# Performance work log

Hardware: AMD Instinct MI355X
Metric: run time of the kernel (lower is better)

## Reference

```python
import jax, jax.numpy as jnp
import numpy as np

LAMBDA_SOFTMAX = 9.0
EPS = 1e-8


def _l2norm(x, axis):
    # matches torch l2norm: x / (sqrt(sum(x^2)+eps) + eps)
    n = jnp.sqrt(jnp.sum(x * x, axis=axis, keepdims=True) + EPS) + EPS
    return x / n


def setup_inputs() -> dict:
    key = jax.random.key(0)
    k1, k2, k3, k4 = jax.random.split(key, 4)
    n_img, n_cap, n_reg, n_words, d = 128, 128, 36, 48, 1024
    return {
        "img_emb": jax.random.normal(k1, (n_img, n_reg, d), jnp.float32),
        "img_mean": jax.random.normal(k2, (n_img, d), jnp.float32),
        "cap_emb": jax.random.normal(k3, (n_cap, n_words, d), jnp.float32),
        "cap_mean": jax.random.normal(k4, (n_cap, d), jnp.float32),
    }


def reference(img_emb, img_mean, cap_emb, cap_mean):
    # img_emb: [I, R, D]; cap_emb: [C, W, D]
    n_reg = img_emb.shape[1]
    n_words = cap_emb.shape[1]
    # global similarities g[c, i]
    g = cap_mean @ img_mean.T
    # raw dot products S[c, i, r, w] = img_emb[i, r] . cap_emb[c, w]
    S = jnp.einsum('ird,cwd->cirw', img_emb, cap_emb)

    # ---- t2i branch: query=cap (w), context=img (r) ----
    # original attn [i, r, w]: leaky -> l2norm over w -> softmax over r
    a = jax.nn.leaky_relu(S, 0.1)
    a = _l2norm(a, axis=3)
    a = jax.nn.softmax(LAMBDA_SOFTMAX * a, axis=2)
    ra = g[:, :, None, None] * a
    ra = ra / jnp.sum(ra, axis=2, keepdims=True)  # renormalize over source (r)
    # t2i_sim[c, i] = mean_w sum_r ra * S  (since weightedContext.cap = ra contracted with S)
    t2i = jnp.einsum('cirw,cirw->ci', ra, S) / n_words

    # ---- i2t branch: query=img (r), context=cap (w) ----
    # original attn [i, w, r]: leaky -> l2norm over r -> softmax over w
    b = jax.nn.leaky_relu(S, 0.1)
    b = _l2norm(b, axis=2)
    b = jax.nn.softmax(LAMBDA_SOFTMAX * b, axis=3)
    rb = g[:, :, None, None] * b
    rb = rb / jnp.sum(rb, axis=3, keepdims=True)  # renormalize over source (w)
    i2t = jnp.einsum('cirw,cirw->ci', rb, S) / n_reg

    # original returns [n_image, n_caption] (columns appended per caption)
    return (t2i + i2t).T
```

## Files before the change

kernel.cpp:

```cpp
#include <hip/hip_runtime.h>
#include <hip/hip_bf16.h>


#define EPSF 1e-8f
#define LAMF 9.0f

constexpr int IN = 128, CN = 128, RN = 36, WN = 48, DN = 1024;
constexpr size_t NIMG = (size_t)IN * RN * DN;

constexpr int AROWS = 4 * RN;
constexpr int BROWS = 4 * WN;
constexpr int TROWS = AROWS + BROWS;
constexpr int BUFB  = TROWS * 64;

using short8 = __attribute__((ext_vector_type(8))) short;
using f32x4  = __attribute__((ext_vector_type(4))) float;

__device__ __forceinline__ float leaky(float x) { return x > 0.f ? x : 0.1f * x; }

__device__ __forceinline__ unsigned short f2bf(float f) {
    unsigned int b = __float_as_uint(f);
    b += 0x7FFFu + ((b >> 16) & 1u);
    return (unsigned short)(b >> 16);
}

__device__ __forceinline__ void gld_lds16(const unsigned short* g, void* l) {
    __builtin_amdgcn_global_load_lds(
        (const __attribute__((address_space(1))) unsigned int*)g,
        (__attribute__((address_space(3))) unsigned int*)l,
        16, 0, 0);
}

__global__ void cvt_bf16(const float* __restrict__ in, unsigned short* __restrict__ out, int n4) {
    int idx = blockIdx.x * blockDim.x + threadIdx.x;
    if (idx >= n4) return;
    float4 v = ((const float4*)in)[idx];
    ushort4 o;
    o.x = f2bf(v.x); o.y = f2bf(v.y); o.z = f2bf(v.z); o.w = f2bf(v.w);
    ((ushort4*)out)[idx] = o;
}

__global__ __launch_bounds__(768, 6) void scan_mfma(
    const unsigned short* __restrict__ wsb,
    float* __restrict__ out)
{
    __shared__ __align__(16) unsigned char smem[61824];
    float (*sS)[RN][WN + 1] = (float (*)[RN][WN + 1])smem;
    float* sncol = (float*)(smem + 56448);
    float* snrow = (float*)(smem + 57984);
    float* scw   = (float*)(smem + 59136);
    float* scr   = (float*)(smem + 60672);

    const int t    = threadIdx.x;
    const int lane = t & 63;
    const int wid  = t >> 6;
    const int lr   = lane & 15;
    const int lg   = lane >> 4;
    const int wrt  = wid % 3;
    const int wct  = wid / 3;

    const int bi = blockIdx.x;
    const int bc = blockIdx.y;

    unsigned int soff[2];
#pragma unroll
    for (int j = 0; j < 2; ++j) {
        int g = j * 768 + t;
        int row = g >> 2, cg = g & 3;
        int sg = cg ^ ((row >> 1) & 3);
        unsigned int off;
        if (row < AROWS)
            off = (unsigned int)((bi * AROWS + row) << 10) + sg * 8;
        else
            off = (unsigned int)NIMG + (unsigned int)((bc * BROWS + (row - AROWS)) << 10) + sg * 8;
        soff[j] = off;
    }

    const int glo = ((lg ^ ((lr >> 1) & 3)) << 4);
    const int aoff = (wrt * 48 + lr) * 64 + glo;
    const int boff = (AROWS + wct * 48 + lr) * 64 + glo;

    f32x4 acc[3][3];
#pragma unroll
    for (int rt = 0; rt < 3; ++rt)
#pragma unroll
        for (int ct = 0; ct < 3; ++ct) acc[rt][ct] = (f32x4)(0.f);

    auto stage = [&](int bsel, int d0) {
        char* bufp = (char*)smem + bsel * BUFB;
        gld_lds16(wsb + soff[0] + d0, bufp + wid * 1024);
        if (t < 576)
            gld_lds16(wsb + soff[1] + d0, bufp + 12288 + wid * 1024);
    };

    stage(0, 0);

    for (int ch = 0; ch < 32; ++ch) {
        __builtin_amdgcn_s_barrier();
        if (ch < 31) {
            stage((ch & 1) ^ 1, (ch + 1) * 32);
            if (wid < 9) asm volatile("s_waitcnt vmcnt(2)" ::: "memory");
            else         asm volatile("s_waitcnt vmcnt(1)" ::: "memory");
        } else {
            asm volatile("s_waitcnt vmcnt(0)" ::: "memory");
        }
        __builtin_amdgcn_s_barrier();
        __builtin_amdgcn_sched_barrier(0);

        const char* bufp = (const char*)smem + (ch & 1) * BUFB;
        const char* ap = bufp + aoff;
        const char* bp = bufp + boff;
        short8 a0 = *(const short8*)(ap);
        short8 a1 = *(const short8*)(ap + 1024);
        short8 a2 = *(const short8*)(ap + 2048);
        short8 b0 = *(const short8*)(bp);
        short8 b1 = *(const short8*)(bp + 1024);
        short8 b2 = *(const short8*)(bp + 2048);

        __builtin_amdgcn_s_setprio(1);
        acc[0][0] = __builtin_amdgcn_mfma_f32_16x16x32_bf16(a0, b0, acc[0][0], 0, 0, 0);
        acc[0][1] = __builtin_amdgcn_mfma_f32_16x16x32_bf16(a0, b1, acc[0][1], 0, 0, 0);
        acc[0][2] = __builtin_amdgcn_mfma_f32_16x16x32_bf16(a0, b2, acc[0][2], 0, 0, 0);
        acc[1][0] = __builtin_amdgcn_mfma_f32_16x16x32_bf16(a1, b0, acc[1][0], 0, 0, 0);
        acc[1][1] = __builtin_amdgcn_mfma_f32_16x16x32_bf16(a1, b1, acc[1][1], 0, 0, 0);
        acc[1][2] = __builtin_amdgcn_mfma_f32_16x16x32_bf16(a1, b2, acc[1][2], 0, 0, 0);
        acc[2][0] = __builtin_amdgcn_mfma_f32_16x16x32_bf16(a2, b0, acc[2][0], 0, 0, 0);
        acc[2][1] = __builtin_amdgcn_mfma_f32_16x16x32_bf16(a2, b1, acc[2][1], 0, 0, 0);
        acc[2][2] = __builtin_amdgcn_mfma_f32_16x16x32_bf16(a2, b2, acc[2][2], 0, 0, 0);
        __builtin_amdgcn_s_setprio(0);
    }
    __syncthreads();

#pragma unroll
    for (int r = 0; r < 2; ++r) {
        if (r == 1 && t < 8) {
            float s1 = 0.f, s2 = 0.f;
            for (int w = 0; w < WN; ++w) s1 += scw[t * WN + w];
            for (int rr = 0; rr < RN; ++rr) s2 += scr[t * RN + rr];
            out[(size_t)(bi * 4 + (t >> 2)) * CN + (bc * 4 + (t & 3))] =
                s1 / (float)WN + s2 / (float)RN;
        }
#pragma unroll
        for (int rt = 0; rt < 3; ++rt)
#pragma unroll
            for (int reg = 0; reg < 4; ++reg) {
                int lrow = wrt * 48 + rt * 16 + lg * 4 + reg;
                int ii = lrow / 36;
                if ((ii >> 1) == r) {
                    int tile = (ii & 1) * 4 + wct;
                    int rin = lrow - ii * 36;
#pragma unroll
                    for (int ct = 0; ct < 3; ++ct)
                        sS[tile][rin][ct * 16 + lr] = acc[rt][ct][reg];
                }
            }
        __syncthreads();

        if (t < 8 * WN) {
            int tile = t / WN, w = t % WN;
            float ss = 0.f;
            for (int rr = 0; rr < RN; ++rr) { float l = leaky(sS[tile][rr][w]); ss = fmaf(l, l, ss); }
            sncol[t] = LAMF / (sqrtf(ss + EPSF) + EPSF);
        }
        if (t < 8 * RN) {
            int tile = t / RN, rr = t % RN;
            float ss = 0.f;
            for (int w = 0; w < WN; ++w) { float l = leaky(sS[tile][rr][w]); ss = fmaf(l, l, ss); }
            snrow[t] = LAMF / (sqrtf(ss + EPSF) + EPSF);
        }
        __syncthreads();

        if (t < 8 * RN) {
            int tile = t / RN, rr = t % RN;
            const float* Sr = sS[tile][rr];
            const float* ic = sncol + tile * WN;
            float se = 0.f, sw = 0.f;
            for (int w = 0; w < WN; ++w) {
                float s = Sr[w];
                float e = __expf(leaky(s) * ic[w]);
                se += e;
                sw = fmaf(e, s, sw);
            }
            scr[t] = sw / se;
        }
        if (t < 8 * WN) {
            int tile = t / WN, w = t % WN;
            const float* ir = snrow + tile * RN;
            float se = 0.f, sw = 0.f;
            for (int rr = 0; rr < RN; ++rr) {
                float s = sS[tile][rr][w];
                float e = __expf(leaky(s) * ir[rr]);
                se += e;
                sw = fmaf(e, s, sw);
            }
            scw[t] = sw / se;
        }
        __syncthreads();
    }

    if (t < 8) {
        float s1 = 0.f, s2 = 0.f;
        for (int w = 0; w < WN; ++w) s1 += scw[t * WN + w];
        for (int rr = 0; rr < RN; ++rr) s2 += scr[t * RN + rr];
        out[(size_t)(bi * 4 + 2 + (t >> 2)) * CN + (bc * 4 + (t & 3))] =
            s1 / (float)WN + s2 / (float)RN;
    }
}

__global__ __launch_bounds__(256, 4) void scan_fused(
    const float* __restrict__ img_emb, const float* __restrict__ cap_emb,
    float* __restrict__ out)
{
    __shared__ float s_img[48][68];
    __shared__ float s_cap[48][68];
    __shared__ float s_S[RN][WN + 1];
    __shared__ float s_nrow[RN];
    __shared__ float s_ncol[WN];
    __shared__ float s_cw[WN];
    __shared__ float s_cr[RN];

    const int t = threadIdx.x;
    const int c = blockIdx.x & (CN - 1);
    const int i = blockIdx.x >> 7;
    const float* imgB = img_emb + (size_t)i * RN * DN;
    const float* capB = cap_emb + (size_t)c * WN * DN;
    const int ty = t >> 4, tx = t & 15;

    float4 acc[3][3];
#pragma unroll
    for (int a = 0; a < 3; ++a)
#pragma unroll
        for (int b = 0; b < 3; ++b) acc[a][b] = make_float4(0.f, 0.f, 0.f, 0.f);

    for (int d0 = 0; d0 < DN; d0 += 64) {
#pragma unroll
        for (int p = 0; p < 3; ++p) {
            int idx = t + p * 256, row = idx >> 4, col = (idx & 15) << 2;
            float4 v = make_float4(0.f, 0.f, 0.f, 0.f);
            if (row < RN) v = *(const float4*)(imgB + row * DN + d0 + col);
            *(float4*)&s_img[row][col] = v;
        }
#pragma unroll
        for (int p = 0; p < 3; ++p) {
            int idx = t + p * 256, row = idx >> 4, col = (idx & 15) << 2;
            *(float4*)&s_cap[row][col] = *(const float4*)(capB + row * DN + d0 + col);
        }
        __syncthreads();
        for (int d = 0; d < 64; d += 4) {
            float4 a0 = *(float4*)&s_img[ty][d], a1 = *(float4*)&s_img[ty + 16][d], a2 = *(float4*)&s_img[ty + 32][d];
            float4 b0 = *(float4*)&s_cap[tx][d], b1 = *(float4*)&s_cap[tx + 16][d], b2 = *(float4*)&s_cap[tx + 32][d];
#define F4(ac, aa, bb) ac.x=fmaf(aa.x,bb.x,ac.x); ac.y=fmaf(aa.y,bb.y,ac.y); ac.z=fmaf(aa.z,bb.z,ac.z); ac.w=fmaf(aa.w,bb.w,ac.w)
            F4(acc[0][0],a0,b0); F4(acc[0][1],a0,b1); F4(acc[0][2],a0,b2);
            F4(acc[1][0],a1,b0); F4(acc[1][1],a1,b1); F4(acc[1][2],a1,b2);
            F4(acc[2][0],a2,b0); F4(acc[2][1],a2,b1); F4(acc[2][2],a2,b2);
#undef F4
        }
        __syncthreads();
    }
#pragma unroll
    for (int a = 0; a < 3; ++a) {
        int r = ty + 16 * a;
        if (r < RN)
#pragma unroll
            for (int b = 0; b < 3; ++b) {
                float4 v = acc[a][b];
                s_S[r][tx + 16 * b] = (v.x + v.y) + (v.z + v.w);
            }
    }
    __syncthreads();
    if (t < RN) {
        float ss = 0.f;
        for (int w = 0; w < WN; ++w) { float l = leaky(s_S[t][w]); ss = fmaf(l, l, ss); }
        s_nrow[t] = sqrtf(ss + EPSF) + EPSF;
    } else if (t >= 64 && t < 64 + WN) {
        int w = t - 64; float ss = 0.f;
        for (int r = 0; r < RN; ++r) { float l = leaky(s_S[r][w]); ss = fmaf(l, l, ss); }
        s_ncol[w] = sqrtf(ss + EPSF) + EPSF;
    }
    __syncthreads();
    if (t < RN) {
        float se = 0.f, sw = 0.f;
        for (int w = 0; w < WN; ++w) {
            float e = __expf(LAMF * leaky(s_S[t][w]) / s_ncol[w]);
            se += e; sw = fmaf(e, s_S[t][w], sw);
        }
        s_cr[t] = sw / se;
    } else if (t >= 64 && t < 64 + WN) {
        int w = t - 64;
        float se = 0.f, sw = 0.f;
        for (int r = 0; r < RN; ++r) {
            float e = __expf(LAMF * leaky(s_S[r][w]) / s_nrow[r]);
            se += e; sw = fmaf(e, s_S[r][w], sw);
        }
        s_cw[w] = sw / se;
    }
    __syncthreads();
    if (t == 0) {
        float t2i = 0.f, i2t = 0.f;
        for (int w = 0; w < WN; ++w) t2i += s_cw[w];
        for (int r = 0; r < RN; ++r) i2t += s_cr[r];
        out[(size_t)i * CN + c] = t2i / (float)WN + i2t / (float)RN;
    }
}

extern "C" void kernel_launch(void* const* d_in, const int* in_sizes, int n_in,
                              void* d_out, int out_size, void* d_ws, size_t ws_size,
                              hipStream_t stream) {
    const float* img = (const float*)d_in[0];
    const float* cap = (const float*)d_in[2];
    float* out = (float*)d_out;

    const size_t n_img = NIMG;
    const size_t n_cap = (size_t)CN * WN * DN;
    const size_t need  = (n_img + n_cap) * 2;

    if (ws_size >= need) {
        unsigned short* imgh = (unsigned short*)d_ws;
        unsigned short* caph = imgh + n_img;
        int n4i = (int)(n_img / 4), n4c = (int)(n_cap / 4);
        hipLaunchKernelGGL(cvt_bf16, dim3((n4i + 255) / 256), dim3(256), 0, stream, img, imgh, n4i);
        hipLaunchKernelGGL(cvt_bf16, dim3((n4c + 255) / 256), dim3(256), 0, stream, cap, caph, n4c);
        hipLaunchKernelGGL(scan_mfma, dim3(IN / 4, CN / 4), dim3(768), 0, stream, imgh, out);
    } else {
        hipLaunchKernelGGL(scan_fused, dim3(IN * CN), dim3(256), 0, stream, img, cap, out);
    }
}
```

Baseline: 97.27 us.

## Widen MFMA block tile to 4 images by 8 captions

Each block now computes a 4-image by 8-caption tile instead of 4 by 4. Each wave holds a 3x6 accumulator grid, and the shared staging buffer grows to hold 384 caption rows per chunk. This halves the grid in the caption dimension and doubles reuse of the staged image rows, cutting global/LDS traffic per output. In exchange it uses more registers and LDS per block, so fewer blocks fit per CU (launch bounds lowered to 3), and the epilogue runs four passes per block instead of two.

```diff
diff --git a/kernel.cpp b/kernel.cpp
--- a/kernel.cpp
+++ b/kernel.cpp
@@ -9,7 +9,7 @@
 constexpr size_t NIMG = (size_t)IN * RN * DN;
 
 constexpr int AROWS = 4 * RN;
-constexpr int BROWS = 4 * WN;
+constexpr int BROWS = 8 * WN;
 constexpr int TROWS = AROWS + BROWS;
 constexpr int BUFB  = TROWS * 64;
 
@@ -40,11 +40,11 @@
     ((ushort4*)out)[idx] = o;
 }
 
-__global__ __launch_bounds__(768, 6) void scan_mfma(
+__global__ __launch_bounds__(768, 3) void scan_mfma(
     const unsigned short* __restrict__ wsb,
     float* __restrict__ out)
 {
-    __shared__ __align__(16) unsigned char smem[61824];
+    __shared__ __align__(16) unsigned char smem[2 * BUFB];
     float (*sS)[RN][WN + 1] = (float (*)[RN][WN + 1])smem;
     float* sncol = (float*)(smem + 56448);
     float* snrow = (float*)(smem + 57984);
@@ -57,15 +57,15 @@
     const int lr   = lane & 15;
     const int lg   = lane >> 4;
     const int wrt  = wid % 3;
-    const int wct  = wid / 3;
+    const int wcp  = wid / 3;
 
     const int bi = blockIdx.x;
     const int bc = blockIdx.y;
 
-    unsigned int soff[2];
-#pragma unroll
-    for (int j = 0; j < 2; ++j) {
-        int g = j * 768 + t;
+    unsigned int soff[3];
+#pragma unroll
+    for (int j = 0; j < 3; ++j) {
+        int g = (j < 2) ? (j * 768 + t) : (1536 + (t & 1023));
         int row = g >> 2, cg = g & 3;
         int sg = cg ^ ((row >> 1) & 3);
         unsigned int off;
@@ -78,19 +78,20 @@
 
     const int glo = ((lg ^ ((lr >> 1) & 3)) << 4);
     const int aoff = (wrt * 48 + lr) * 64 + glo;
-    const int boff = (AROWS + wct * 48 + lr) * 64 + glo;
-
-    f32x4 acc[3][3];
+    const int boff = (AROWS + wcp * 96 + lr) * 64 + glo;
+
+    f32x4 acc[3][6];
 #pragma unroll
     for (int rt = 0; rt < 3; ++rt)
 #pragma unroll
-        for (int ct = 0; ct < 3; ++ct) acc[rt][ct] = (f32x4)(0.f);
+        for (int ct = 0; ct < 6; ++ct) acc[rt][ct] = (f32x4)(0.f);
 
     auto stage = [&](int bsel, int d0) {
         char* bufp = (char*)smem + bsel * BUFB;
         gld_lds16(wsb + soff[0] + d0, bufp + wid * 1024);
+        gld_lds16(wsb + soff[1] + d0, bufp + 12288 + wid * 1024);
         if (t < 576)
-            gld_lds16(wsb + soff[1] + d0, bufp + 12288 + wid * 1024);
+            gld_lds16(wsb + soff[2] + d0, bufp + 24576 + wid * 1024);
     };
 
     stage(0, 0);
@@ -99,8 +100,8 @@
         __builtin_amdgcn_s_barrier();
         if (ch < 31) {
             stage((ch & 1) ^ 1, (ch + 1) * 32);
-            if (wid < 9) asm volatile("s_waitcnt vmcnt(2)" ::: "memory");
-            else         asm volatile("s_waitcnt vmcnt(1)" ::: "memory");
+            if (wid < 9) asm volatile("s_waitcnt vmcnt(3)" ::: "memory");
+            else         asm volatile("s_waitcnt vmcnt(2)" ::: "memory");
         } else {
             asm volatile("s_waitcnt vmcnt(0)" ::: "memory");
         }
@@ -113,31 +114,28 @@
         short8 a0 = *(const short8*)(ap);
         short8 a1 = *(const short8*)(ap + 1024);
         short8 a2 = *(const short8*)(ap + 2048);
-        short8 b0 = *(const short8*)(bp);
-        short8 b1 = *(const short8*)(bp + 1024);
-        short8 b2 = *(const short8*)(bp + 2048);
+        short8 b[6];
+#pragma unroll
+        for (int ct = 0; ct < 6; ++ct) b[ct] = *(const short8*)(bp + ct * 1024);
 
         __builtin_amdgcn_s_setprio(1);
-        acc[0][0] = __builtin_amdgcn_mfma_f32_16x16x32_bf16(a0, b0, acc[0][0], 0, 0, 0);
-        acc[0][1] = __builtin_amdgcn_mfma_f32_16x16x32_bf16(a0, b1, acc[0][1], 0, 0, 0);
-        acc[0][2] = __builtin_amdgcn_mfma_f32_16x16x32_bf16(a0, b2, acc[0][2], 0, 0, 0);
-        acc[1][0] = __builtin_amdgcn_mfma_f32_16x16x32_bf16(a1, b0, acc[1][0], 0, 0, 0);
-        acc[1][1] = __builtin_amdgcn_mfma_f32_16x16x32_bf16(a1, b1, acc[1][1], 0, 0, 0);
-        acc[1][2] = __builtin_amdgcn_mfma_f32_16x16x32_bf16(a1, b2, acc[1][2], 0, 0, 0);
-        acc[2][0] = __builtin_amdgcn_mfma_f32_16x16x32_bf16(a2, b0, acc[2][0], 0, 0, 0);
-        acc[2][1] = __builtin_amdgcn_mfma_f32_16x16x32_bf16(a2, b1, acc[2][1], 0, 0, 0);
-        acc[2][2] = __builtin_amdgcn_mfma_f32_16x16x32_bf16(a2, b2, acc[2][2], 0, 0, 0);
+#pragma unroll
+        for (int ct = 0; ct < 6; ++ct) {
+            acc[0][ct] = __builtin_amdgcn_mfma_f32_16x16x32_bf16(a0, b[ct], acc[0][ct], 0, 0, 0);
+            acc[1][ct] = __builtin_amdgcn_mfma_f32_16x16x32_bf16(a1, b[ct], acc[1][ct], 0, 0, 0);
+            acc[2][ct] = __builtin_amdgcn_mfma_f32_16x16x32_bf16(a2, b[ct], acc[2][ct], 0, 0, 0);
+        }
         __builtin_amdgcn_s_setprio(0);
     }
     __syncthreads();
 
 #pragma unroll
-    for (int r = 0; r < 2; ++r) {
-        if (r == 1 && t < 8) {
+    for (int r = 0; r < 4; ++r) {
+        if (r > 0 && t < 8) {
             float s1 = 0.f, s2 = 0.f;
             for (int w = 0; w < WN; ++w) s1 += scw[t * WN + w];
             for (int rr = 0; rr < RN; ++rr) s2 += scr[t * RN + rr];
-            out[(size_t)(bi * 4 + (t >> 2)) * CN + (bc * 4 + (t & 3))] =
+            out[(size_t)(bi * 4 + (r - 1)) * CN + (bc * 8 + t)] =
                 s1 / (float)WN + s2 / (float)RN;
         }
 #pragma unroll
@@ -146,12 +144,14 @@
             for (int reg = 0; reg < 4; ++reg) {
                 int lrow = wrt * 48 + rt * 16 + lg * 4 + reg;
                 int ii = lrow / 36;
-                if ((ii >> 1) == r) {
-                    int tile = (ii & 1) * 4 + wct;
+                if (ii == r) {
                     int rin = lrow - ii * 36;
 #pragma unroll
-                    for (int ct = 0; ct < 3; ++ct)
-                        sS[tile][rin][ct * 16 + lr] = acc[rt][ct][reg];
+                    for (int ct = 0; ct < 6; ++ct) {
+                        int tile = wcp * 2 + (ct >= 3 ? 1 : 0);
+                        int col = (ct % 3) * 16 + lr;
+                        sS[tile][rin][col] = acc[rt][ct][reg];
+                    }
                 }
             }
         __syncthreads();
@@ -202,7 +202,7 @@
         float s1 = 0.f, s2 = 0.f;
         for (int w = 0; w < WN; ++w) s1 += scw[t * WN + w];
         for (int rr = 0; rr < RN; ++rr) s2 += scr[t * RN + rr];
-        out[(size_t)(bi * 4 + 2 + (t >> 2)) * CN + (bc * 4 + (t & 3))] =
+        out[(size_t)(bi * 4 + 3) * CN + (bc * 8 + t)] =
             s1 / (float)WN + s2 / (float)RN;
     }
 }
@@ -320,7 +320,7 @@
         int n4i = (int)(n_img / 4), n4c = (int)(n_cap / 4);
         hipLaunchKernelGGL(cvt_bf16, dim3((n4i + 255) / 256), dim3(256), 0, stream, img, imgh, n4i);
         hipLaunchKernelGGL(cvt_bf16, dim3((n4c + 255) / 256), dim3(256), 0, stream, cap, caph, n4c);
-        hipLaunchKernelGGL(scan_mfma, dim3(IN / 4, CN / 4), dim3(768), 0, stream, imgh, out);
+        hipLaunchKernelGGL(scan_mfma, dim3(IN / 4, CN / 8), dim3(768), 0, stream, imgh, out);
     } else {
         hipLaunchKernelGGL(scan_fused, dim3(IN * CN), dim3(256), 0, stream, img, cap, out);
     }
```

New measurement: 110.0 us. 13.1% more time.
